# Performance work log

Hardware: AMD Instinct MI355X
Metric: run time of the kernel (lower is better)

## Reference

```python
import jax, jax.numpy as jnp
import numpy as np


def setup_inputs() -> dict:
    key = jax.random.key(0)
    k1, k2 = jax.random.split(key)
    z = jax.random.normal(k1, (16, 128, 32, 32), dtype=jnp.float32)
    codes = jax.random.normal(k2, (8, 512, 16), dtype=jnp.float32)  # [latent_dim, num_codes, channel_dim]
    return {"z": z, "codes": codes}


def reference(z, codes):
    L, K, D = codes.shape          # latent_dim, num_codes, channel_dim
    B, C, H, W = z.shape           # C == L * D
    # permute to channels-last and split channels into (L, D)
    h = jnp.transpose(z, (0, 2, 3, 1)).reshape(B, H, W, L, D)
    # pairwise L2 distances via ||h||^2 - 2 h.W + ||W||^2 (avoids materializing [B,H,W,L,K,D])
    h2 = jnp.sum(h * h, axis=-1)                      # [B,H,W,L]
    w2 = jnp.sum(codes * codes, axis=-1)              # [L,K]
    cross = jnp.einsum('bhwld,lkd->bhwlk', h, codes)  # [B,H,W,L,K]
    d2 = h2[..., None] - 2.0 * cross + w2[None, None, None]
    distances = jnp.sqrt(jnp.maximum(d2, 1e-12))      # [B,H,W,L,K]
    # softmin over codes == softmax of negated distances
    probs = jax.nn.softmax(-distances, axis=4)
    soft_symbols = jnp.einsum('bhwlk,lkd->bhwld', probs, codes).reshape(B, H, W, C)
    # hard assignment: nearest code per latent dim
    idxes = jnp.argmin(distances, axis=4)             # [B,H,W,L]
    hard_symbols = codes[jnp.arange(L), idxes]        # [B,H,W,L,D]
    hard_symbols = hard_symbols.reshape(B, H, W, C)
    return (soft_symbols, hard_symbols, idxes)
```

## Files before the change

### kernel.cpp

```cpp
#include <hip/hip_runtime.h>
#include <hip/hip_bf16.h>

typedef float  f32x4  __attribute__((ext_vector_type(4)));
typedef short  s16x8  __attribute__((ext_vector_type(8)));
typedef __bf16 bf16x8 __attribute__((ext_vector_type(8)));

namespace {
constexpr int BHW = 16384, L = 8, K = 512, D = 16, HW = 1024, CH = 128;
constexpr int TPB = 512;
constexpr int PPB = 128;
constexpr size_t WS_CA_ELEMS = (size_t)L * K * 32;

__device__ __forceinline__ f32x4 mfma16(s16x8 a, s16x8 b, f32x4 c) {
  return __builtin_amdgcn_mfma_f32_16x16x32_bf16(
      __builtin_bit_cast(bf16x8, a), __builtin_bit_cast(bf16x8, b), c, 0, 0, 0);
}
__device__ __forceinline__ unsigned short bfh(float x) {
  return __builtin_bit_cast(unsigned short, __float2bfloat16(x));
}
__device__ __forceinline__ float bf2f(unsigned short u) {
  return __bfloat162float(__builtin_bit_cast(__hip_bfloat16, u));
}

__global__ void repack(const float* __restrict__ codes,
                       unsigned short* __restrict__ cA, float* __restrict__ w2g) {
  int i = blockIdx.x * 256 + threadIdx.x;
  const float* c = codes + (size_t)i * D;
  float s = 0.f;
  #pragma unroll
  for (int d = 0; d < D; ++d) s = fmaf(c[d], c[d], s);
  w2g[i] = s;
  int l = i >> 9, k = i & (K - 1);
  int ck = k >> 5, kloc = k & 31, g = kloc >> 3, w = kloc & 7, t = w >> 2, r = w & 3;
  int prow = ck * 32 + t * 16 + g * 4 + r;
  unsigned short* dst = cA + ((size_t)l * K + prow) * 32;
  #pragma unroll
  for (int d = 0; d < D; ++d) {
    unsigned short hi = bfh(c[d]);
    dst[d] = hi; dst[16 + d] = bfh(c[d] - bf2f(hi));
  }
}

__global__ __launch_bounds__(TPB, 5) void enc_mfma(
    const float* __restrict__ z,
    const float* __restrict__ codes,
    const unsigned short* __restrict__ cA,
    const float* __restrict__ w2g,
    float* __restrict__ out)
{
  __shared__ unsigned short cBh[8192];
  __shared__ unsigned short cBl[8192];
  __shared__ float w2s[K];
  __shared__ unsigned short hH[128][16], hL[128][16];
  __shared__ float h2s[128];
  __shared__ float ssum[8][16];
  __shared__ int   bks[8][16];

  const int tid  = threadIdx.x;
  const int l    = blockIdx.y;
  const int bx   = blockIdx.x;
  const int bimg = bx >> 3;
  const int yx0  = (bx & 7) * 128;

  float* hstg = (float*)cBh;
  {
    const int i = tid & 127, dc = tid >> 7;
    #pragma unroll
    for (int it = 0; it < 4; ++it) {
      int d = dc + it * 4;
      hstg[i * 17 + d] = z[((size_t)(bimg * CH + l * D + d)) * HW + yx0 + i];
    }
  }
  __syncthreads();
  if (tid < 128) {
    float h[16]; float h2 = 0.f;
    #pragma unroll
    for (int d = 0; d < 16; ++d) h[d] = hstg[tid * 17 + d];
    #pragma unroll
    for (int d = 0; d < 16; ++d) h2 = fmaf(h[d], h[d], h2);
    h2s[tid] = h2;
    #pragma unroll
    for (int d = 0; d < 16; ++d) {
      unsigned short hi = bfh(h[d]);
      hH[tid][d] = hi;
      hL[tid][d] = bfh(h[d] - bf2f(hi));
    }
  }
  __syncthreads();
  {
    int k = tid, ck = k >> 5, kloc = k & 31, g = kloc >> 3, w = kloc & 7, t = w >> 2, r = w & 3;
    int prow = ck * 32 + t * 16 + g * 4 + r;
    const s16x8* src = (const s16x8*)(cA + ((size_t)l * K + prow) * 32);
    s16x8 h0 = src[0], h1 = src[1], l0 = src[2], l1 = src[3];
    int base = (ck * 4 + g) * 128 + w;
    #pragma unroll
    for (int d = 0; d < 8; ++d) {
      cBh[base + d * 8]       = (unsigned short)h0[d];
      cBl[base + d * 8]       = (unsigned short)l0[d];
      cBh[base + (d + 8) * 8] = (unsigned short)h1[d];
      cBl[base + (d + 8) * 8] = (unsigned short)l1[d];
    }
    w2s[k] = w2g[l * K + k];
  }
  __syncthreads();

  const int wv   = __builtin_amdgcn_readfirstlane(tid >> 6);
  const int lane = tid & 63;
  const int cl   = lane & 15;
  const int g    = lane >> 4;
  const int pw   = wv * 16;
  const int myp  = pw + cl;

  s16x8 B1 = *(const s16x8*)&hH[myp][(g & 1) * 8];
  s16x8 B2 = *(const s16x8*)&hL[myp][(g & 1) * 8];
  const float h2 = h2s[myp];

  const s16x8* Ab = (const s16x8*)(cA + (size_t)l * K * 32) + (cl * 4 + g);

  float m2k = 1e30f, m2bk = 1e30f, s = 0.f;
  f32x4 pv0 = {0.f, 0.f, 0.f, 0.f}, pv1 = {0.f, 0.f, 0.f, 0.f};

  #pragma unroll 2
  for (int ck = 0; ck < 16; ++ck) {
    s16x8 A0 = Ab[ck * 128];
    s16x8 A1 = Ab[ck * 128 + 64];
    s16x8 Bh = *(const s16x8*)&cBh[(ck * 4 + g) * 128 + cl * 8];
    s16x8 Bl = *(const s16x8*)&cBl[(ck * 4 + g) * 128 + cl * 8];

    f32x4 T0 = {0.f, 0.f, 0.f, 0.f}, T1 = {0.f, 0.f, 0.f, 0.f};
    T0 = mfma16(A0, B1, T0); T0 = mfma16(A0, B2, T0);
    T1 = mfma16(A1, B1, T1); T1 = mfma16(A1, B2, T1);

    f32x4 W0 = *(const f32x4*)&w2s[ck * 32 + 8 * g];
    f32x4 W1 = *(const f32x4*)&w2s[ck * 32 + 8 * g + 4];

    float wt[8];
    #pragma unroll
    for (int t = 0; t < 2; ++t) {
      #pragma unroll
      for (int r = 0; r < 4; ++r) {
        float T  = t ? T1[r] : T0[r];
        float Wk = t ? W1[r] : W0[r];
        float d2 = fmaf(-2.f, T, h2) + Wk;
        d2 = fmaxf(d2, 1e-12f);
        int kloc = ck * 32 + 8 * g + t * 4 + r;
        float key = __int_as_float((__float_as_int(d2) & 0xFFFFFE00) | kloc);
        m2bk = __builtin_amdgcn_fmed3f(key, m2k, m2bk);
        m2k  = fminf(m2k, key);
        float dist = __builtin_amdgcn_sqrtf(d2);
        float w = __builtin_amdgcn_exp2f(dist * -1.44269504088896340736f);
        s += w;
        wt[t * 4 + r] = w;
      }
    }
    s16x8 PA;
    #pragma unroll
    for (int j = 0; j < 8; ++j) PA[j] = (short)bfh(wt[j]);
    pv0 = mfma16(PA, Bh, pv0);
    pv1 = mfma16(PA, Bl, pv1);
  }
  f32x4 pv = pv0 + pv1;

  #pragma unroll
  for (int off = 16; off < 64; off <<= 1) {
    s += __shfl_xor(s, off);
    float m2o  = __shfl_xor(m2k, off);
    float m2bo = __shfl_xor(m2bk, off);
    m2bk = fminf(fminf(m2bk, m2bo), fmaxf(m2k, m2o));
    m2k  = fminf(m2k, m2o);
  }
  int ka = __float_as_int(m2k) & 511;
  float d2min = __int_as_float(__float_as_int(m2k)  & 0xFFFFFE00);
  float d2sec = __int_as_float(__float_as_int(m2bk) & 0xFFFFFE00);
  bool trig = (d2sec - d2min) < 0.02f;

  if (lane < 16) { ssum[wv][lane] = s; bks[wv][lane] = ka; }

  unsigned long long mask = __ballot(lane < 16 && trig);
  while (mask) {
    int pl = __ffsll((long long)mask) - 1; mask &= mask - 1;
    float hh[16];
    #pragma unroll
    for (int d = 0; d < 16; ++d)
      hh[d] = z[((size_t)(bimg * CH + l * D + d)) * HW + yx0 + pw + pl];
    float h2x = h2s[pw + pl];
    float bm = 1e30f; int bkk = 0;
    for (int rnd = 0; rnd < 8; ++rnd) {
      int k = rnd * 64 + lane;
      const float* cr = codes + ((size_t)l * K + k) * D;
      float cross = 0.f;
      #pragma unroll
      for (int d = 0; d < 16; ++d) cross = fmaf(hh[d], cr[d], cross);
      float d2 = (h2x - 2.f * cross) + w2g[l * K + k];
      d2 = fmaxf(d2, 1e-12f);
      float dist = sqrtf(d2);
      if (dist < bm) { bm = dist; bkk = k; }
    }
    #pragma unroll
    for (int off = 1; off < 64; off <<= 1) {
      float bo = __shfl_xor(bm, off); int ko = __shfl_xor(bkk, off);
      if (bo < bm || (bo == bm && ko < bkk)) { bm = bo; bkk = ko; }
    }
    if (lane == 0) bks[wv][pl] = bkk;
  }

  const int pg0 = bimg * HW + yx0;
  f32x4 sv = *(const f32x4*)&ssum[wv][g * 4];
  #pragma unroll
  for (int r = 0; r < 4; ++r) {
    float inv = __builtin_amdgcn_rcpf(sv[r]);
    out[(size_t)(pg0 + pw + g * 4 + r) * CH + l * D + cl] = pv[r] * inv;
  }
  int kk = bks[wv][cl];
  float4 cv = *(const float4*)&codes[((size_t)l * K + kk) * D + g * 4];
  *(float4*)&out[(size_t)BHW * CH + (size_t)(pg0 + pw + cl) * CH + l * D + g * 4] = cv;
  if (lane < 16)
    out[(size_t)2 * BHW * CH + (size_t)(pg0 + pw + cl) * L + l] = (float)kk;
}
}

extern "C" void kernel_launch(void* const* d_in, const int* in_sizes, int n_in,
                              void* d_out, int out_size, void* d_ws, size_t ws_size,
                              hipStream_t stream) {
  const float* z     = (const float*)d_in[0];
  const float* codes = (const float*)d_in[1];
  float* out         = (float*)d_out;
  unsigned short* cA = (unsigned short*)d_ws;
  float* w2g         = (float*)((char*)d_ws + WS_CA_ELEMS * 2);

  repack<<<dim3(L * K / 256), 256, 0, stream>>>(codes, cA, w2g);
  dim3 grid(BHW / PPB, L);
  enc_mfma<<<grid, TPB, 0, stream>>>(z, codes, cA, w2g, out);
}
```

Measured before the change: 73.43 us.

## Process two 16-pixel groups per wave to reuse code fragments across pixels

```diff
diff --git a/kernel.cpp b/kernel.cpp
--- a/kernel.cpp
+++ b/kernel.cpp
@@ -8,7 +8,7 @@
 namespace {
 constexpr int BHW = 16384, L = 8, K = 512, D = 16, HW = 1024, CH = 128;
 constexpr int TPB = 512;
-constexpr int PPB = 128;
+constexpr int PPB = 256;
 constexpr size_t WS_CA_ELEMS = (size_t)L * K * 32;
 
 __device__ __forceinline__ f32x4 mfma16(s16x8 a, s16x8 b, f32x4 c) {
@@ -41,66 +41,33 @@
   }
 }
 
-__global__ __launch_bounds__(TPB, 5) void enc_mfma(
+__global__ __launch_bounds__(TPB, 4) void enc_mfma(
     const float* __restrict__ z,
     const float* __restrict__ codes,
     const unsigned short* __restrict__ cA,
     const float* __restrict__ w2g,
     float* __restrict__ out)
 {
-  __shared__ unsigned short cBh[8192];
-  __shared__ unsigned short cBl[8192];
+  __shared__ short cB[2][8192];
   __shared__ float w2s[K];
-  __shared__ unsigned short hH[128][16], hL[128][16];
-  __shared__ float h2s[128];
-  __shared__ float ssum[8][16];
-  __shared__ int   bks[8][16];
+  __shared__ float h2s[PPB];
+  __shared__ float ssum[8][32];
+  __shared__ int   bks[8][32];
 
   const int tid  = threadIdx.x;
   const int l    = blockIdx.y;
   const int bx   = blockIdx.x;
-  const int bimg = bx >> 3;
-  const int yx0  = (bx & 7) * 128;
-
-  float* hstg = (float*)cBh;
+  const int bimg = bx >> 2;
+  const int yx0  = (bx & 3) * PPB;
+
+  float* hstg = (float*)&cB[0][0];
   {
-    const int i = tid & 127, dc = tid >> 7;
-    #pragma unroll
-    for (int it = 0; it < 4; ++it) {
-      int d = dc + it * 4;
+    const int i = tid & 255, dc = tid >> 8;
+    #pragma unroll
+    for (int it = 0; it < 8; ++it) {
+      int d = dc * 8 + it;
       hstg[i * 17 + d] = z[((size_t)(bimg * CH + l * D + d)) * HW + yx0 + i];
     }
-  }
-  __syncthreads();
-  if (tid < 128) {
-    float h[16]; float h2 = 0.f;
-    #pragma unroll
-    for (int d = 0; d < 16; ++d) h[d] = hstg[tid * 17 + d];
-    #pragma unroll
-    for (int d = 0; d < 16; ++d) h2 = fmaf(h[d], h[d], h2);
-    h2s[tid] = h2;
-    #pragma unroll
-    for (int d = 0; d < 16; ++d) {
-      unsigned short hi = bfh(h[d]);
-      hH[tid][d] = hi;
-      hL[tid][d] = bfh(h[d] - bf2f(hi));
-    }
-  }
-  __syncthreads();
-  {
-    int k = tid, ck = k >> 5, kloc = k & 31, g = kloc >> 3, w = kloc & 7, t = w >> 2, r = w & 3;
-    int prow = ck * 32 + t * 16 + g * 4 + r;
-    const s16x8* src = (const s16x8*)(cA + ((size_t)l * K + prow) * 32);
-    s16x8 h0 = src[0], h1 = src[1], l0 = src[2], l1 = src[3];
-    int base = (ck * 4 + g) * 128 + w;
-    #pragma unroll
-    for (int d = 0; d < 8; ++d) {
-      cBh[base + d * 8]       = (unsigned short)h0[d];
-      cBl[base + d * 8]       = (unsigned short)l0[d];
-      cBh[base + (d + 8) * 8] = (unsigned short)h1[d];
-      cBl[base + (d + 8) * 8] = (unsigned short)l1[d];
-    }
-    w2s[k] = w2g[l * K + k];
   }
   __syncthreads();
 
@@ -108,33 +75,57 @@
   const int lane = tid & 63;
   const int cl   = lane & 15;
   const int g    = lane >> 4;
-  const int pw   = wv * 16;
-  const int myp  = pw + cl;
-
-  s16x8 B1 = *(const s16x8*)&hH[myp][(g & 1) * 8];
-  s16x8 B2 = *(const s16x8*)&hL[myp][(g & 1) * 8];
-  const float h2 = h2s[myp];
+  const int pw   = wv * 32;
+
+  if (tid < PPB) {
+    float h2 = 0.f;
+    #pragma unroll
+    for (int d = 0; d < 16; ++d) { float v = hstg[tid * 17 + d]; h2 = fmaf(v, v, h2); }
+    h2s[tid] = h2;
+  }
+  s16x8 B1a, B2a, B1b, B2b;
+  {
+    const int off = (g & 1) * 8;
+    #pragma unroll
+    for (int j = 0; j < 8; ++j) {
+      float va = hstg[(pw + cl) * 17 + off + j];
+      unsigned short ha = bfh(va);
+      B1a[j] = (short)ha; B2a[j] = (short)bfh(va - bf2f(ha));
+      float vb = hstg[(pw + 16 + cl) * 17 + off + j];
+      unsigned short hb = bfh(vb);
+      B1b[j] = (short)hb; B2b[j] = (short)bfh(vb - bf2f(hb));
+    }
+  }
+  __syncthreads();
+  const float h2a = h2s[pw + cl];
+  const float h2b = h2s[pw + 16 + cl];
+
+  {
+    int k = tid, ck = k >> 5, kloc = k & 31, gg = kloc >> 3, w = kloc & 7, t = w >> 2, r = w & 3;
+    int prow = ck * 32 + t * 16 + gg * 4 + r;
+    const s16x8* src = (const s16x8*)(cA + ((size_t)l * K + prow) * 32);
+    s16x8 h0 = src[0], h1 = src[1], l0 = src[2], l1 = src[3];
+    int base = (ck * 4 + gg) * 128 + w;
+    #pragma unroll
+    for (int d = 0; d < 8; ++d) {
+      cB[0][base + d * 8]       = h0[d];
+      cB[1][base + d * 8]       = l0[d];
+      cB[0][base + (d + 8) * 8] = h1[d];
+      cB[1][base + (d + 8) * 8] = l1[d];
+    }
+    w2s[k] = w2g[l * K + k];
+  }
+  __syncthreads();
 
   const s16x8* Ab = (const s16x8*)(cA + (size_t)l * K * 32) + (cl * 4 + g);
 
-  float m2k = 1e30f, m2bk = 1e30f, s = 0.f;
-  f32x4 pv0 = {0.f, 0.f, 0.f, 0.f}, pv1 = {0.f, 0.f, 0.f, 0.f};
-
-  #pragma unroll 2
-  for (int ck = 0; ck < 16; ++ck) {
-    s16x8 A0 = Ab[ck * 128];
-    s16x8 A1 = Ab[ck * 128 + 64];
-    s16x8 Bh = *(const s16x8*)&cBh[(ck * 4 + g) * 128 + cl * 8];
-    s16x8 Bl = *(const s16x8*)&cBl[(ck * 4 + g) * 128 + cl * 8];
-
-    f32x4 T0 = {0.f, 0.f, 0.f, 0.f}, T1 = {0.f, 0.f, 0.f, 0.f};
-    T0 = mfma16(A0, B1, T0); T0 = mfma16(A0, B2, T0);
-    T1 = mfma16(A1, B1, T1); T1 = mfma16(A1, B2, T1);
-
-    f32x4 W0 = *(const f32x4*)&w2s[ck * 32 + 8 * g];
-    f32x4 W1 = *(const f32x4*)&w2s[ck * 32 + 8 * g + 4];
-
-    float wt[8];
+  float m2A = 1e30f, mbA = 1e30f, sA = 0.f;
+  float m2B = 1e30f, mbB = 1e30f, sB = 0.f;
+  f32x4 pva0 = {0,0,0,0}, pva1 = {0,0,0,0}, pvb0 = {0,0,0,0}, pvb1 = {0,0,0,0};
+
+  auto soft8 = [&](f32x4 T0, f32x4 T1, f32x4 W0, f32x4 W1, float h2, int ck,
+                   float& m2, float& m2b, float& s) -> s16x8 {
+    s16x8 PA;
     #pragma unroll
     for (int t = 0; t < 2; ++t) {
       #pragma unroll
@@ -145,38 +136,67 @@
         d2 = fmaxf(d2, 1e-12f);
         int kloc = ck * 32 + 8 * g + t * 4 + r;
         float key = __int_as_float((__float_as_int(d2) & 0xFFFFFE00) | kloc);
-        m2bk = __builtin_amdgcn_fmed3f(key, m2k, m2bk);
-        m2k  = fminf(m2k, key);
+        m2b = __builtin_amdgcn_fmed3f(key, m2, m2b);
+        m2  = fminf(m2, key);
         float dist = __builtin_amdgcn_sqrtf(d2);
         float w = __builtin_amdgcn_exp2f(dist * -1.44269504088896340736f);
         s += w;
-        wt[t * 4 + r] = w;
+        PA[t * 4 + r] = (short)bfh(w);
       }
     }
-    s16x8 PA;
-    #pragma unroll
-    for (int j = 0; j < 8; ++j) PA[j] = (short)bfh(wt[j]);
-    pv0 = mfma16(PA, Bh, pv0);
-    pv1 = mfma16(PA, Bl, pv1);
-  }
-  f32x4 pv = pv0 + pv1;
+    return PA;
+  };
+
+  #pragma unroll 2
+  for (int ck = 0; ck < 16; ++ck) {
+    s16x8 A0 = Ab[ck * 128];
+    s16x8 A1 = Ab[ck * 128 + 64];
+    s16x8 Bh = *(const s16x8*)&cB[0][(ck * 4 + g) * 128 + cl * 8];
+    s16x8 Bl = *(const s16x8*)&cB[1][(ck * 4 + g) * 128 + cl * 8];
+    f32x4 W0 = *(const f32x4*)&w2s[ck * 32 + 8 * g];
+    f32x4 W1 = *(const f32x4*)&w2s[ck * 32 + 8 * g + 4];
+
+    f32x4 T0a = {0,0,0,0}, T1a = {0,0,0,0}, T0b = {0,0,0,0}, T1b = {0,0,0,0};
+    T0a = mfma16(A0, B1a, T0a); T0a = mfma16(A0, B2a, T0a);
+    T1a = mfma16(A1, B1a, T1a); T1a = mfma16(A1, B2a, T1a);
+    T0b = mfma16(A0, B1b, T0b); T0b = mfma16(A0, B2b, T0b);
+    T1b = mfma16(A1, B1b, T1b); T1b = mfma16(A1, B2b, T1b);
+
+    s16x8 PAa = soft8(T0a, T1a, W0, W1, h2a, ck, m2A, mbA, sA);
+    pva0 = mfma16(PAa, Bh, pva0);
+    pva1 = mfma16(PAa, Bl, pva1);
+    s16x8 PAb = soft8(T0b, T1b, W0, W1, h2b, ck, m2B, mbB, sB);
+    pvb0 = mfma16(PAb, Bh, pvb0);
+    pvb1 = mfma16(PAb, Bl, pvb1);
+  }
+  f32x4 pva = pva0 + pva1;
+  f32x4 pvb = pvb0 + pvb1;
 
   #pragma unroll
   for (int off = 16; off < 64; off <<= 1) {
-    s += __shfl_xor(s, off);
-    float m2o  = __shfl_xor(m2k, off);
-    float m2bo = __shfl_xor(m2bk, off);
-    m2bk = fminf(fminf(m2bk, m2bo), fmaxf(m2k, m2o));
-    m2k  = fminf(m2k, m2o);
-  }
-  int ka = __float_as_int(m2k) & 511;
-  float d2min = __int_as_float(__float_as_int(m2k)  & 0xFFFFFE00);
-  float d2sec = __int_as_float(__float_as_int(m2bk) & 0xFFFFFE00);
-  bool trig = (d2sec - d2min) < 0.02f;
-
-  if (lane < 16) { ssum[wv][lane] = s; bks[wv][lane] = ka; }
-
-  unsigned long long mask = __ballot(lane < 16 && trig);
+    sA += __shfl_xor(sA, off);
+    float mo = __shfl_xor(m2A, off), mbo = __shfl_xor(mbA, off);
+    mbA = fminf(fminf(mbA, mbo), fmaxf(m2A, mo));
+    m2A = fminf(m2A, mo);
+    sB += __shfl_xor(sB, off);
+    float mo2 = __shfl_xor(m2B, off), mbo2 = __shfl_xor(mbB, off);
+    mbB = fminf(fminf(mbB, mbo2), fmaxf(m2B, mo2));
+    m2B = fminf(m2B, mo2);
+  }
+  int kaA = __float_as_int(m2A) & 511;
+  int kaB = __float_as_int(m2B) & 511;
+  bool trigA = (__int_as_float(__float_as_int(mbA) & 0xFFFFFE00) -
+                __int_as_float(__float_as_int(m2A) & 0xFFFFFE00)) < 0.02f;
+  bool trigB = (__int_as_float(__float_as_int(mbB) & 0xFFFFFE00) -
+                __int_as_float(__float_as_int(m2B) & 0xFFFFFE00)) < 0.02f;
+
+  if (lane < 16) {
+    ssum[wv][lane] = sA;      bks[wv][lane] = kaA;
+    ssum[wv][16 + lane] = sB; bks[wv][16 + lane] = kaB;
+  }
+
+  unsigned long long mask = __ballot(lane < 16 && trigA) |
+                            (__ballot(lane < 16 && trigB) << 16);
   while (mask) {
     int pl = __ffsll((long long)mask) - 1; mask &= mask - 1;
     float hh[16];
@@ -204,18 +224,25 @@
     if (lane == 0) bks[wv][pl] = bkk;
   }
 
+  __syncthreads();
   const int pg0 = bimg * HW + yx0;
-  f32x4 sv = *(const f32x4*)&ssum[wv][g * 4];
+  f32x4 svA = *(const f32x4*)&ssum[wv][g * 4];
+  f32x4 svB = *(const f32x4*)&ssum[wv][16 + g * 4];
   #pragma unroll
   for (int r = 0; r < 4; ++r) {
-    float inv = __builtin_amdgcn_rcpf(sv[r]);
-    out[(size_t)(pg0 + pw + g * 4 + r) * CH + l * D + cl] = pv[r] * inv;
-  }
-  int kk = bks[wv][cl];
-  float4 cv = *(const float4*)&codes[((size_t)l * K + kk) * D + g * 4];
-  *(float4*)&out[(size_t)BHW * CH + (size_t)(pg0 + pw + cl) * CH + l * D + g * 4] = cv;
-  if (lane < 16)
-    out[(size_t)2 * BHW * CH + (size_t)(pg0 + pw + cl) * L + l] = (float)kk;
+    out[(size_t)(pg0 + pw + g * 4 + r) * CH + l * D + cl]      = pva[r] * __builtin_amdgcn_rcpf(svA[r]);
+    out[(size_t)(pg0 + pw + 16 + g * 4 + r) * CH + l * D + cl] = pvb[r] * __builtin_amdgcn_rcpf(svB[r]);
+  }
+  int kkA = bks[wv][cl];
+  int kkB = bks[wv][16 + cl];
+  float4 cvA = *(const float4*)&codes[((size_t)l * K + kkA) * D + g * 4];
+  float4 cvB = *(const float4*)&codes[((size_t)l * K + kkB) * D + g * 4];
+  *(float4*)&out[(size_t)BHW * CH + (size_t)(pg0 + pw + cl) * CH + l * D + g * 4]      = cvA;
+  *(float4*)&out[(size_t)BHW * CH + (size_t)(pg0 + pw + 16 + cl) * CH + l * D + g * 4] = cvB;
+  if (lane < 16) {
+    out[(size_t)2 * BHW * CH + (size_t)(pg0 + pw + cl) * L + l]      = (float)kkA;
+    out[(size_t)2 * BHW * CH + (size_t)(pg0 + pw + 16 + cl) * L + l] = (float)kkB;
+  }
 }
 }
 
```

Result: faster. 63.38 us (-13.7%).
